# Kernel tuning notes

Hardware: AMD Instinct MI355X
Metric: run time of the kernel (lower is better)

## Reference

```python
import jax, jax.numpy as jnp
import numpy as np

B = 4
N_PER_B = 65536
N = B * N_PER_B
GROUP_SIZE = 64
ORDER = 9  # min bits to cover grid size 512
C0, C1, C2 = 64, 128, 128


def hilbert_encode(coors, order):
    """Skilling AxesToTranspose, vectorized over N points, 3 dims -> int32 code."""
    n = 3
    X = [coors[:, i].astype(jnp.int32) for i in range(n)]
    M = 1 << (order - 1)
    Q = M
    while Q > 1:
        P = Q - 1
        for i in range(n):
            cond = (X[i] & Q) != 0
            if i == 0:
                X[0] = jnp.where(cond, X[0] ^ P, X[0])
            else:
                t = (X[0] ^ X[i]) & P
                x0 = jnp.where(cond, X[0] ^ P, X[0] ^ t)
                xi = jnp.where(cond, X[i], X[i] ^ t)
                X[0], X[i] = x0, xi
        Q >>= 1
    for i in range(1, n):
        X[i] = X[i] ^ X[i - 1]
    t = jnp.zeros_like(X[0])
    Q = M
    while Q > 1:
        t = jnp.where((X[n - 1] & Q) != 0, t ^ (Q - 1), t)
        Q >>= 1
    X = [x ^ t for x in X]
    # interleave transposed bits MSB-first: code has 3*order bits (27 < 31, fits int32)
    code = jnp.zeros_like(X[0])
    for b in range(order - 1, -1, -1):
        for i in range(n):
            code = (code << 1) | ((X[i] >> b) & 1)
    return code


def _mapping_indices(vox_coors):
    """Two Hilbert orderings (normal + reversed coord axes); per-batch stable grouping."""
    batch = vox_coors[:, 0]
    c1 = vox_coors[:, 1:4]
    c2 = vox_coors[:, 3:0:-1]  # [0,3,2,1] reverse of the xyz columns
    code1 = hilbert_encode(c1, ORDER)
    code2 = hilbert_encode(c2, ORDER)
    ind1 = jnp.lexsort((code1, batch))  # batch-major, curve-order minor
    ind2 = jnp.lexsort((code2, batch))
    inv1 = jnp.argsort(ind1)
    ind12 = inv1[ind2]  # maps ordering-1 arrangement to ordering-2 arrangement
    return ind1, ind12


def _block(p, x, params):
    """VoxFormer-style block: center pts per group, pos-encode, gate feats, local attn, FFN."""
    Wpos, bpos, Wq, Wk, Wv, Wo, Wout = params
    C = Wq.shape[0]
    gs = GROUP_SIZE
    pg = p.reshape(-1, gs, 3)
    e = (pg - pg.mean(axis=1, keepdims=True)).reshape(-1, 3) @ Wpos + bpos  # [N,C]
    h = (x * e).reshape(-1, gs, C)  # [G,gs,C]
    q, k, v = h @ Wq, h @ Wk, h @ Wv
    scores = jnp.einsum('gqc,gkc->gqk', q, k) / jnp.sqrt(jnp.asarray(C, q.dtype))
    attn = jax.nn.softmax(scores, axis=-1)
    o = jnp.einsum('gqk,gkc->gqc', attn, v).reshape(-1, C) @ Wo
    return jax.nn.relu(o) @ Wout  # [N,C_out]


def setup_inputs() -> dict:
    key = jax.random.key(0)
    ks = jax.random.split(key, 20)
    bcol = jnp.repeat(jnp.arange(B, dtype=jnp.int32), N_PER_B)
    z = jax.random.randint(ks[0], (N,), 0, 64, dtype=jnp.int32)
    y = jax.random.randint(ks[1], (N,), 0, 512, dtype=jnp.int32)
    x = jax.random.randint(ks[2], (N,), 0, 512, dtype=jnp.int32)
    vox_coors = jnp.stack([bcol, z, y, x], axis=1)
    vox_numbs = jnp.full((B,), N_PER_B, dtype=jnp.int32)
    vox_feats = jax.random.normal(ks[3], (N, C0), dtype=jnp.float32)
    pts_coors = jax.random.normal(ks[4], (N, 3), dtype=jnp.float32)
    s = lambda k, shape: jax.random.normal(k, shape, dtype=jnp.float32) / np.float32(np.sqrt(shape[0]))
    return dict(
        vox_numbs=vox_numbs, vox_coors=vox_coors, vox_feats=vox_feats, pts_coors=pts_coors,
        Wpos1=s(ks[5], (3, C0)), bpos1=jnp.zeros((C0,), jnp.float32),
        Wq1=s(ks[6], (C0, C0)), Wk1=s(ks[7], (C0, C0)), Wv1=s(ks[8], (C0, C0)),
        Wo1=s(ks[9], (C0, C0)), Wout1=s(ks[10], (C0, C1)),
        Wpos2=s(ks[11], (3, C1)), bpos2=jnp.zeros((C1,), jnp.float32),
        Wq2=s(ks[12], (C1, C1)), Wk2=s(ks[13], (C1, C1)), Wv2=s(ks[14], (C1, C1)),
        Wo2=s(ks[15], (C1, C1)), Wout2=s(ks[16], (C1, C2)),
    )


def reference(vox_numbs, vox_coors, vox_feats, pts_coors,
              Wpos1, bpos1, Wq1, Wk1, Wv1, Wo1, Wout1,
              Wpos2, bpos2, Wq2, Wk2, Wv2, Wo2, Wout2):
    ind1, ind12 = _mapping_indices(vox_coors)
    params = ((Wpos1, bpos1, Wq1, Wk1, Wv1, Wo1, Wout1),
              (Wpos2, bpos2, Wq2, Wk2, Wv2, Wo2, Wout2))
    for ind, prm in zip((ind1, ind12), params):
        vox_feats = vox_feats[ind]
        pts_coors = pts_coors[ind]
        vox_coors = vox_coors[ind]
        vox_feats = _block(pts_coors, vox_feats, prm)
    return vox_feats, pts_coors, vox_coors, vox_numbs
```

## Files before the change

### kernel.cpp

```cpp
#include <hip/hip_runtime.h>

using u64 = unsigned long long;
typedef _Float16 f16;
using f16x8 = __attribute__((ext_vector_type(8))) _Float16;
using f16x4 = __attribute__((ext_vector_type(4))) _Float16;
using f32x4 = __attribute__((ext_vector_type(4))) float;

__device__ __forceinline__ int hilbert3(int X0, int X1, int X2) {
  #pragma unroll
  for (int Q = 256; Q > 1; Q >>= 1) {
    const int P = Q - 1;
    if (X0 & Q) X0 ^= P;
    int t1 = (X0 ^ X1) & P;
    if (X1 & Q) X0 ^= P; else { X0 ^= t1; X1 ^= t1; }
    int t2 = (X0 ^ X2) & P;
    if (X2 & Q) X0 ^= P; else { X0 ^= t2; X2 ^= t2; }
  }
  X1 ^= X0;
  X2 ^= X1;
  int t = 0;
  #pragma unroll
  for (int Q = 256; Q > 1; Q >>= 1) if (X2 & Q) t ^= (Q - 1);
  X0 ^= t; X1 ^= t; X2 ^= t;
  int code = 0;
  #pragma unroll
  for (int b = 8; b >= 0; b--)
    code = (code << 3) | (((X0 >> b) & 1) << 2) | (((X1 >> b) & 1) << 1) | ((X2 >> b) & 1);
  return code;
}

__global__ void encode_keys(const int* __restrict__ vox, u64* __restrict__ k1,
                            u64* __restrict__ k2, int n) {
  int i = blockIdx.x * blockDim.x + threadIdx.x;
  if (i >= n) return;
  int4 c = ((const int4*)vox)[i];
  unsigned code1 = (unsigned)hilbert3(c.y, c.z, c.w);
  unsigned code2 = (unsigned)hilbert3(c.w, c.z, c.y);
  u64 bb = ((u64)(unsigned)c.x << 45);
  k1[i] = bb | ((u64)code1 << 18) | (unsigned)i;
  k2[i] = bb | ((u64)code2 << 18) | (unsigned)i;
}

__device__ __forceinline__ void cswap(u64& a, u64& b, bool up) {
  if ((a > b) == up) { u64 t = a; a = b; b = t; }
}

__global__ __launch_bounds__(1024) void bitonic_tile_sort(u64* __restrict__ keys, int n) {
  keys += (size_t)blockIdx.y * n;
  __shared__ u64 s[2048];
  const int base = blockIdx.x * 2048;
  s[threadIdx.x]        = keys[base + threadIdx.x];
  s[threadIdx.x + 1024] = keys[base + threadIdx.x + 1024];
  __syncthreads();
  for (int k = 2; k <= 2048; k <<= 1) {
    for (int j = k >> 1; j >= 1; j >>= 1) {
      const int t = threadIdx.x;
      const int i = ((t & ~(j - 1)) << 1) | (t & (j - 1));
      const int l = i | j;
      const bool up = (((base + i) & k) == 0);
      u64 a = s[i], b = s[l];
      if ((a > b) == up) { s[i] = b; s[l] = a; }
      __syncthreads();
    }
  }
  keys[base + threadIdx.x]        = s[threadIdx.x];
  keys[base + threadIdx.x + 1024] = s[threadIdx.x + 1024];
}

__global__ void bitonic_g1(u64* __restrict__ keys, int j, int k, int n) {
  keys += (size_t)blockIdx.y * n;
  const int t = blockIdx.x * blockDim.x + threadIdx.x;
  const int i = ((t & ~(j - 1)) << 1) | (t & (j - 1));
  const int l = i | j;
  const bool up = ((i & k) == 0);
  u64 a = keys[i], b = keys[l];
  if ((a > b) == up) { keys[i] = b; keys[l] = a; }
}

__global__ void bitonic_g2(u64* __restrict__ keys, int j2, int k, int n) {
  keys += (size_t)blockIdx.y * n;
  const int t = blockIdx.x * blockDim.x + threadIdx.x;
  const int i = ((t & ~(j2 - 1)) << 2) | (t & (j2 - 1));
  const bool up = ((i & k) == 0);
  u64 x0 = keys[i], x1 = keys[i + j2], x2 = keys[i + 2 * j2], x3 = keys[i + 3 * j2];
  cswap(x0, x2, up); cswap(x1, x3, up);
  cswap(x0, x1, up); cswap(x2, x3, up);
  keys[i] = x0; keys[i + j2] = x1; keys[i + 2 * j2] = x2; keys[i + 3 * j2] = x3;
}

__global__ void bitonic_g3(u64* __restrict__ keys, int j4, int k, int n) {
  keys += (size_t)blockIdx.y * n;
  const int t = blockIdx.x * blockDim.x + threadIdx.x;
  const int i = ((t & ~(j4 - 1)) << 3) | (t & (j4 - 1));
  const bool up = ((i & k) == 0);
  u64 x[8];
  #pragma unroll
  for (int m = 0; m < 8; m++) x[m] = keys[i + m * j4];
  #pragma unroll
  for (int m = 0; m < 4; m++) cswap(x[m], x[m + 4], up);
  cswap(x[0], x[2], up); cswap(x[1], x[3], up);
  cswap(x[4], x[6], up); cswap(x[5], x[7], up);
  #pragma unroll
  for (int m = 0; m < 8; m += 2) cswap(x[m], x[m + 1], up);
  #pragma unroll
  for (int m = 0; m < 8; m++) keys[i + m * j4] = x[m];
}

__global__ __launch_bounds__(1024) void bitonic_tile_merge(u64* __restrict__ keys, int k, int n) {
  keys += (size_t)blockIdx.y * n;
  __shared__ u64 s[2048];
  const int base = blockIdx.x * 2048;
  s[threadIdx.x]        = keys[base + threadIdx.x];
  s[threadIdx.x + 1024] = keys[base + threadIdx.x + 1024];
  __syncthreads();
  const bool up = ((base & k) == 0);
  for (int j = 1024; j >= 1; j >>= 1) {
    const int t = threadIdx.x;
    const int i = ((t & ~(j - 1)) << 1) | (t & (j - 1));
    const int l = i | j;
    u64 a = s[i], b = s[l];
    if ((a > b) == up) { s[i] = b; s[l] = a; }
    __syncthreads();
  }
  keys[base + threadIdx.x]        = s[threadIdx.x];
  keys[base + threadIdx.x + 1024] = s[threadIdx.x + 1024];
}

__global__ void extract_inv_k(const u64* __restrict__ keys, int* __restrict__ ind,
                              int* __restrict__ inv, int n) {
  int t = blockIdx.x * blockDim.x + threadIdx.x;
  if (t >= n) return;
  int s = (int)(keys[t] & 0x3FFFFULL);
  ind[t] = s;
  inv[s] = t;
}

__global__ void make_g2_k(const u64* __restrict__ keys, const int* __restrict__ inv1,
                          int* __restrict__ ind2, int* __restrict__ g2, int n) {
  int t = blockIdx.x * blockDim.x + threadIdx.x;
  if (t >= n) return;
  int s = (int)(keys[t] & 0x3FFFFULL);
  ind2[t] = s;
  g2[t] = inv1[s];
}

__global__ void prep_all(const float* __restrict__ Wq1, const float* __restrict__ Wk1,
                         const float* __restrict__ Wv1, const float* __restrict__ Wo1,
                         const float* __restrict__ Wout1,
                         const float* __restrict__ Wq2, const float* __restrict__ Wk2,
                         const float* __restrict__ Wv2, const float* __restrict__ Wo2,
                         const float* __restrict__ Wout2,
                         f16* __restrict__ A1a, f16* __restrict__ A2a, f16* __restrict__ A3a,
                         f16* __restrict__ A1b, f16* __restrict__ A2b, f16* __restrict__ A3b) {
  const int idx = blockIdx.x * blockDim.x + threadIdx.x;
  if (idx < 4096) {
    const int a = idx >> 6, b = idx & 63;
    float s1 = 0.f, s2 = 0.f;
    for (int c = 0; c < 64; c++) {
      s1 = fmaf(Wq1[b * 64 + c], Wk1[a * 64 + c], s1);
      s2 = fmaf(Wv1[b * 64 + c], Wo1[c * 64 + a], s2);
    }
    A1a[idx] = (f16)(s1 * 0.125f);
    A2a[idx] = (f16)s2;
  }
  if (idx < 8192) {
    const int o = idx >> 6, c = idx & 63;
    A3a[idx] = (f16)Wout1[c * 128 + o];
  }
  {
    const int a = idx >> 7, b = idx & 127;
    float s1 = 0.f, s2 = 0.f;
    for (int c = 0; c < 128; c++) {
      s1 = fmaf(Wq2[b * 128 + c], Wk2[a * 128 + c], s1);
      s2 = fmaf(Wv2[b * 128 + c], Wo2[c * 128 + a], s2);
    }
    A1b[idx] = (f16)(s1 * 0.08838834764831845f);
    A2b[idx] = (f16)s2;
    A3b[idx] = (f16)Wout2[b * 128 + a];
  }
}


template<int M, int K, int AMODE>
__device__ __forceinline__ void gemmT(const f16* __restrict__ Ag, const f16* __restrict__ lA,
                                      const f16* __restrict__ lB, int w, int lane,
                                      f32x4 (&acc)[M / 64][4]) {
  constexpr int CT = M / 64;
  const int lr = lane & 15, lk = lane >> 4;
  #pragma unroll
  for (int ks = 0; ks < K / 32; ks++) {
    const int k0 = ks * 32 + lk * 8;
    f16x8 Af[CT];
    #pragma unroll
    for (int ct = 0; ct < CT; ct++) {
      const int c = lr + (w * CT + ct) * 16;
      if (AMODE == 0) {
        Af[ct] = *(const f16x8*)(Ag + (size_t)c * K + k0);
      } else if (AMODE == 1) {
        Af[ct] = *(const f16x8*)((const char*)lA + (((c * K + k0) * 2) ^ ((c & 7) << 4)));
      } else {
        f16x8 a;
        #pragma unroll
        for (int e = 0; e < 8; e++) {
          const int j = k0 + e;
          a[e] = *(const f16*)((const char*)lA + (((j * M + c) * 2) ^ ((j & 7) << 4)));
        }
        Af[ct] = a;
      }
    }
    f16x8 Bf[4];
    #pragma unroll
    for (int qt = 0; qt < 4; qt++) {
      const int q = lr + qt * 16;
      Bf[qt] = *(const f16x8*)((const char*)lB + (((q * K + k0) * 2) ^ ((q & 7) << 4)));
    }
    #pragma unroll
    for (int ct = 0; ct < CT; ct++)
      #pragma unroll
      for (int qt = 0; qt < 4; qt++)
        acc[ct][qt] = __builtin_amdgcn_mfma_f32_16x16x32_f16(Af[ct], Bf[qt], acc[ct][qt], 0, 0, 0);
  }
}

template<int M, bool RELU>
__device__ __forceinline__ void storeT16(f16* __restrict__ dst, int w, int lane,
                                         const f32x4 (&acc)[M / 64][4]) {
  constexpr int CT = M / 64;
  #pragma unroll
  for (int ct = 0; ct < CT; ct++)
    #pragma unroll
    for (int qt = 0; qt < 4; qt++) {
      const int q = (lane & 15) + qt * 16;
      const int c0 = (w * CT + ct) * 16 + (lane >> 4) * 4;
      f16x4 v;
      #pragma unroll
      for (int r = 0; r < 4; r++) {
        float x = acc[ct][qt][r];
        if (RELU) x = fmaxf(x, 0.f);
        v[r] = (f16)x;
      }
      *(f16x4*)((char*)dst + (((q * M + c0) * 2) ^ ((q & 7) << 4))) = v;
    }
}

template<int C, bool X16, bool OUT16>
__global__ __launch_bounds__(256, 3) void block_mfma(
    const int* __restrict__ idx_p, const int* __restrict__ idx_x,
    const float* __restrict__ pts, const void* __restrict__ xsrc,
    const float* __restrict__ Wpos, const float* __restrict__ bpos,
    const f16* __restrict__ A1, const f16* __restrict__ A2, const f16* __restrict__ A3,
    void* __restrict__ outp) {
  extern __shared__ char smem[];
  f16*   bufH = (f16*)smem;
  f16*   bufT = bufH + 64 * C;
  float* scF  = (float*)(bufT + 64 * C);

  const int g = blockIdx.x;
  const int t = threadIdx.x;
  const int lane = t & 63;
  const int w = t >> 6;

  {
    const int qr = t & 63;
    const int spr = idx_p[g * 64 + qr];
    float mx = pts[spr * 3 + 0], my = pts[spr * 3 + 1], mz = pts[spr * 3 + 2];
    #pragma unroll
    for (int o = 32; o > 0; o >>= 1) {
      mx += __shfl_xor(mx, o); my += __shfl_xor(my, o); mz += __shfl_xor(mz, o);
    }
    mx *= (1.f / 64.f); my *= (1.f / 64.f); mz *= (1.f / 64.f);

    const int q = t >> 2, qq = t & 3;
    const int sp = idx_p[g * 64 + q];
    const float d0 = pts[sp * 3 + 0] - mx;
    const float d1 = pts[sp * 3 + 1] - my;
    const float d2 = pts[sp * 3 + 2] - mz;
    const int sx = idx_x[g * 64 + q];
    #pragma unroll
    for (int i = 0; i < C / 32; i++) {
      const int c0 = qq * (C / 4) + i * 8;
      float xv[8];
      if (X16) {
        f16x8 xr = *(const f16x8*)((const f16*)xsrc + (size_t)sx * C + c0);
        #pragma unroll
        for (int j = 0; j < 8; j++) xv[j] = (float)xr[j];
      } else {
        float4 x0 = *(const float4*)((const float*)xsrc + (size_t)sx * C + c0);
        float4 x1 = *(const float4*)((const float*)xsrc + (size_t)sx * C + c0 + 4);
        xv[0] = x0.x; xv[1] = x0.y; xv[2] = x0.z; xv[3] = x0.w;
        xv[4] = x1.x; xv[5] = x1.y; xv[6] = x1.z; xv[7] = x1.w;
      }
      f16x8 hv;
      #pragma unroll
      for (int jj = 0; jj < 8; jj += 4) {
        const float4 w0 = *(const float4*)(Wpos + 0 * C + c0 + jj);
        const float4 w1 = *(const float4*)(Wpos + 1 * C + c0 + jj);
        const float4 w2 = *(const float4*)(Wpos + 2 * C + c0 + jj);
        const float4 bb = *(const float4*)(bpos + c0 + jj);
        hv[jj + 0] = (f16)(xv[jj + 0] * fmaf(d0, w0.x, fmaf(d1, w1.x, fmaf(d2, w2.x, bb.x))));
        hv[jj + 1] = (f16)(xv[jj + 1] * fmaf(d0, w0.y, fmaf(d1, w1.y, fmaf(d2, w2.y, bb.y))));
        hv[jj + 2] = (f16)(xv[jj + 2] * fmaf(d0, w0.z, fmaf(d1, w1.z, fmaf(d2, w2.z, bb.z))));
        hv[jj + 3] = (f16)(xv[jj + 3] * fmaf(d0, w0.w, fmaf(d1, w1.w, fmaf(d2, w2.w, bb.w))));
      }
      *(f16x8*)((char*)bufH + (((q * C + c0) * 2) ^ ((q & 7) << 4))) = hv;
    }
  }
  __syncthreads();

  {
    f32x4 acc[C / 64][4] = {};
    gemmT<C, C, 0>(A1, nullptr, bufH, w, lane, acc);
    storeT16<C, false>(bufT, w, lane, acc);
  }
  __syncthreads();

  {
    f32x4 acc[1][4] = {};
    gemmT<64, C, 1>(nullptr, bufH, bufT, w, lane, acc);
    #pragma unroll
    for (int qt = 0; qt < 4; qt++) {
      const int q = (lane & 15) + qt * 16;
      const int j0 = w * 16 + (lane >> 4) * 4;
      *(f32x4*)((char*)scF + (((q * 64 + j0) * 4) ^ ((q & 7) << 4))) = acc[0][qt];
    }
  }
  __syncthreads();

  {
    const int q = t >> 2, qq = t & 3;
    float v[16];
    float mxv = -3.0e38f;
    #pragma unroll
    for (int i = 0; i < 4; i++) {
      f32x4 x = *(const f32x4*)((const char*)scF + (((q * 64 + qq * 16 + i * 4) * 4) ^ ((q & 7) << 4)));
      v[i * 4 + 0] = x[0]; v[i * 4 + 1] = x[1]; v[i * 4 + 2] = x[2]; v[i * 4 + 3] = x[3];
      mxv = fmaxf(mxv, fmaxf(fmaxf(x[0], x[1]), fmaxf(x[2], x[3])));
    }
    mxv = fmaxf(mxv, __shfl_xor(mxv, 1));
    mxv = fmaxf(mxv, __shfl_xor(mxv, 2));
    float s = 0.f;
    #pragma unroll
    for (int i = 0; i < 16; i++) { v[i] = __expf(v[i] - mxv); s += v[i]; }
    s += __shfl_xor(s, 1);
    s += __shfl_xor(s, 2);
    const float inv = 1.f / s;
    __syncthreads();
    f16* at = (f16*)scF;
    #pragma unroll
    for (int hhalf = 0; hhalf < 2; hhalf++) {
      f16x8 pk;
      #pragma unroll
      for (int j = 0; j < 8; j++) pk[j] = (f16)(v[hhalf * 8 + j] * inv);
      *(f16x8*)((char*)at + (((q * 64 + qq * 16 + hhalf * 8) * 2) ^ ((q & 7) << 4))) = pk;
    }
  }
  __syncthreads();

  {
    f32x4 acc[C / 64][4] = {};
    gemmT<C, 64, 2>(nullptr, bufH, (const f16*)scF, w, lane, acc);
    storeT16<C, false>(bufT, w, lane, acc);
  }
  __syncthreads();

  {
    f32x4 acc[C / 64][4] = {};
    gemmT<C, C, 0>(A2, nullptr, bufT, w, lane, acc);
    storeT16<C, true>(bufH, w, lane, acc);
  }
  __syncthreads();

  {
    f32x4 acc[2][4] = {};
    gemmT<128, C, 0>(A3, nullptr, bufH, w, lane, acc);
    #pragma unroll
    for (int ct = 0; ct < 2; ct++)
      #pragma unroll
      for (int qt = 0; qt < 4; qt++) {
        const int q = (lane & 15) + qt * 16;
        const int o0 = (w * 2 + ct) * 16 + (lane >> 4) * 4;
        const size_t row = (size_t)g * 64 + q;
        if (OUT16) {
          f16x4 v;
          #pragma unroll
          for (int r = 0; r < 4; r++) v[r] = (f16)acc[ct][qt][r];
          *(f16x4*)((f16*)outp + row * 128 + o0) = v;
        } else {
          *(f32x4*)((float*)outp + row * 128 + o0) = acc[ct][qt];
        }
      }
  }
}

__global__ void finalize_k(const int* __restrict__ ind2, const float* __restrict__ pts,
                           const int* __restrict__ vox, const int* __restrict__ numbs,
                           float* __restrict__ out_pts, float* __restrict__ out_vox,
                           float* __restrict__ out_nb, int n, int B) {
  int t = blockIdx.x * blockDim.x + threadIdx.x;
  if (t < n) {
    const int s = ind2[t];
    out_pts[t * 3 + 0] = pts[s * 3 + 0];
    out_pts[t * 3 + 1] = pts[s * 3 + 1];
    out_pts[t * 3 + 2] = pts[s * 3 + 2];
    const int4 v = ((const int4*)vox)[s];
    out_vox[t * 4 + 0] = (float)v.x;
    out_vox[t * 4 + 1] = (float)v.y;
    out_vox[t * 4 + 2] = (float)v.z;
    out_vox[t * 4 + 3] = (float)v.w;
  }
  if (t < B) out_nb[t] = (float)numbs[t];
}

extern "C" void kernel_launch(void* const* d_in, const int* in_sizes, int n_in,
                              void* d_out, int out_size, void* d_ws, size_t ws_size,
                              hipStream_t stream) {
  const int*   vox_numbs = (const int*)d_in[0];
  const int*   vox_coors = (const int*)d_in[1];
  const float* vox_feats = (const float*)d_in[2];
  const float* pts_coors = (const float*)d_in[3];
  const float* Wpos1 = (const float*)d_in[4];
  const float* bpos1 = (const float*)d_in[5];
  const float* Wq1   = (const float*)d_in[6];
  const float* Wk1   = (const float*)d_in[7];
  const float* Wv1   = (const float*)d_in[8];
  const float* Wo1   = (const float*)d_in[9];
  const float* Wout1 = (const float*)d_in[10];
  const float* Wpos2 = (const float*)d_in[11];
  const float* bpos2 = (const float*)d_in[12];
  const float* Wq2   = (const float*)d_in[13];
  const float* Wk2   = (const float*)d_in[14];
  const float* Wv2   = (const float*)d_in[15];
  const float* Wo2   = (const float*)d_in[16];
  const float* Wout2 = (const float*)d_in[17];

  const int B = in_sizes[0];
  const int n = in_sizes[1] / 4;
  const int ngrp = n / 64;

  char* w = (char*)d_ws;
  auto alloc = [&](size_t bytes) {
    char* p = w;
    w += (bytes + 255) & ~(size_t)255;
    return p;
  };
  u64* keys    = (u64*)alloc((size_t)2 * n * 8);
  int* ind1    = (int*)alloc((size_t)n * 4);
  int* ind2    = (int*)alloc((size_t)n * 4);
  int* inv1    = (int*)alloc((size_t)n * 4);
  int* g2      = (int*)alloc((size_t)n * 4);
  f16* A1a     = (f16*)alloc(64 * 64 * 2);
  f16* A2a     = (f16*)alloc(64 * 64 * 2);
  f16* A3a     = (f16*)alloc(128 * 64 * 2);
  f16* A1b     = (f16*)alloc(128 * 128 * 2);
  f16* A2b     = (f16*)alloc(128 * 128 * 2);
  f16* A3b     = (f16*)alloc(128 * 128 * 2);
  f16* feats1  = (f16*)alloc((size_t)n * 128 * 2);
  u64* keys2   = keys + n;

  float* out_feats = (float*)d_out;
  float* out_pts   = out_feats + (size_t)n * 128;
  float* out_vox   = out_pts + (size_t)n * 3;
  float* out_nb    = out_vox + (size_t)n * 4;

  auto f64k  = block_mfma<64,  false, true>;
  auto f128k = block_mfma<128, true,  false>;
  hipFuncSetAttribute((const void*)f64k,  hipFuncAttributeMaxDynamicSharedMemorySize, 65536);
  hipFuncSetAttribute((const void*)f128k, hipFuncAttributeMaxDynamicSharedMemorySize, 65536);

  encode_keys<<<(n + 255) / 256, 256, 0, stream>>>(vox_coors, keys, keys2, n);
  prep_all<<<64, 256, 0, stream>>>(Wq1, Wk1, Wv1, Wo1, Wout1, Wq2, Wk2, Wv2, Wo2, Wout2,
                                   A1a, A2a, A3a, A1b, A2b, A3b);

  {
    const dim3 gt(n / 2048, 2);
    const dim3 g1(n / 512, 2), g2d(n / 1024, 2), g3d(n / 2048, 2);
    bitonic_tile_sort<<<gt, 1024, 0, stream>>>(keys, n);
    for (int k = 4096; k <= n; k <<= 1) {
      int levels = 0;
      for (int j = k >> 1; j >= 2048; j >>= 1) levels++;
      int j = k >> 1;
      while (levels >= 3) {
        bitonic_g3<<<g3d, 256, 0, stream>>>(keys, j >> 2, k, n);
        j >>= 3; levels -= 3;
      }
      if (levels == 2) { bitonic_g2<<<g2d, 256, 0, stream>>>(keys, j >> 1, k, n); j >>= 2; levels = 0; }
      else if (levels == 1) { bitonic_g1<<<g1, 256, 0, stream>>>(keys, j, k, n); j >>= 1; levels = 0; }
      bitonic_tile_merge<<<gt, 1024, 0, stream>>>(keys, k, n);
    }
  }
  extract_inv_k<<<(n + 255) / 256, 256, 0, stream>>>(keys, ind1, inv1, n);
  make_g2_k<<<(n + 255) / 256, 256, 0, stream>>>(keys2, inv1, ind2, g2, n);

  block_mfma<64, false, true><<<ngrp, 256, 32768, stream>>>(
      ind1, ind1, pts_coors, vox_feats, Wpos1, bpos1, A1a, A2a, A3a, feats1);
  block_mfma<128, true, false><<<ngrp, 256, 49152, stream>>>(
      ind2, g2, pts_coors, feats1, Wpos2, bpos2, A1b, A2b, A3b, out_feats);

  finalize_k<<<(n + 255) / 256, 256, 0, stream>>>(ind2, pts_coors, vox_coors, vox_numbs,
                                                  out_pts, out_vox, out_nb, n, B);
}
```

Baseline: 321.7 us.

## Fuse key encoding into 4096-tile sort, radix-16 merges, fp16 scores, pre-gathered points

Hilbert key encoding now happens inside a 4096-element shared-memory tile sort, and the global merge steps use a 16-way bitonic kernel. Both changes cut the number of kernel launches and global passes. Point coordinates are gathered once into sorted order and reused by both blocks, and the finalize work is folded into the g2 construction kernel. Inside the block kernel, the attention scores are stored as fp16 instead of fp32, which shrinks shared memory and allows higher occupancy (launch bounds raised from 3 to 4). The A1 fragments and the x loads are also hoisted into registers, at the cost of more register pressure and fp16 rounding of the scores.

```diff
diff --git a/kernel.cpp b/kernel.cpp
--- a/kernel.cpp
+++ b/kernel.cpp
@@ -29,52 +29,50 @@
   return code;
 }
 
-__global__ void encode_keys(const int* __restrict__ vox, u64* __restrict__ k1,
-                            u64* __restrict__ k2, int n) {
-  int i = blockIdx.x * blockDim.x + threadIdx.x;
-  if (i >= n) return;
-  int4 c = ((const int4*)vox)[i];
-  unsigned code1 = (unsigned)hilbert3(c.y, c.z, c.w);
-  unsigned code2 = (unsigned)hilbert3(c.w, c.z, c.y);
-  u64 bb = ((u64)(unsigned)c.x << 45);
-  k1[i] = bb | ((u64)code1 << 18) | (unsigned)i;
-  k2[i] = bb | ((u64)code2 << 18) | (unsigned)i;
-}
-
 __device__ __forceinline__ void cswap(u64& a, u64& b, bool up) {
   if ((a > b) == up) { u64 t = a; a = b; b = t; }
 }
 
-__global__ __launch_bounds__(1024) void bitonic_tile_sort(u64* __restrict__ keys, int n) {
-  keys += (size_t)blockIdx.y * n;
-  __shared__ u64 s[2048];
-  const int base = blockIdx.x * 2048;
-  s[threadIdx.x]        = keys[base + threadIdx.x];
-  s[threadIdx.x + 1024] = keys[base + threadIdx.x + 1024];
-  __syncthreads();
-  for (int k = 2; k <= 2048; k <<= 1) {
+__global__ __launch_bounds__(1024) void sort_tile0(const int* __restrict__ vox,
+                                                   u64* __restrict__ keys, int n) {
+  __shared__ u64 s[4096];
+  const int base = blockIdx.x * 4096;
+  const int which = blockIdx.y;
+  u64* kout = keys + (size_t)which * n;
+  #pragma unroll
+  for (int m = 0; m < 4; m++) {
+    const int i = base + threadIdx.x + m * 1024;
+    int4 c = ((const int4*)vox)[i];
+    unsigned code = which == 0 ? (unsigned)hilbert3(c.y, c.z, c.w)
+                               : (unsigned)hilbert3(c.w, c.z, c.y);
+    s[threadIdx.x + m * 1024] = ((u64)(unsigned)c.x << 45) | ((u64)code << 18) | (unsigned)i;
+  }
+  __syncthreads();
+  for (int k = 2; k <= 4096; k <<= 1) {
     for (int j = k >> 1; j >= 1; j >>= 1) {
-      const int t = threadIdx.x;
-      const int i = ((t & ~(j - 1)) << 1) | (t & (j - 1));
-      const int l = i | j;
-      const bool up = (((base + i) & k) == 0);
-      u64 a = s[i], b = s[l];
-      if ((a > b) == up) { s[i] = b; s[l] = a; }
+      #pragma unroll
+      for (int m = 0; m < 2; m++) {
+        const int p = threadIdx.x + m * 1024;
+        const int i = ((p & ~(j - 1)) << 1) | (p & (j - 1));
+        const bool up = (((base + i) & k) == 0);
+        u64 a = s[i], b = s[i | j];
+        if ((a > b) == up) { s[i] = b; s[i | j] = a; }
+      }
       __syncthreads();
     }
   }
-  keys[base + threadIdx.x]        = s[threadIdx.x];
-  keys[base + threadIdx.x + 1024] = s[threadIdx.x + 1024];
+  #pragma unroll
+  for (int m = 0; m < 4; m++)
+    kout[base + threadIdx.x + m * 1024] = s[threadIdx.x + m * 1024];
 }
 
 __global__ void bitonic_g1(u64* __restrict__ keys, int j, int k, int n) {
   keys += (size_t)blockIdx.y * n;
   const int t = blockIdx.x * blockDim.x + threadIdx.x;
   const int i = ((t & ~(j - 1)) << 1) | (t & (j - 1));
-  const int l = i | j;
   const bool up = ((i & k) == 0);
-  u64 a = keys[i], b = keys[l];
-  if ((a > b) == up) { keys[i] = b; keys[l] = a; }
+  u64 a = keys[i], b = keys[i | j];
+  if ((a > b) == up) { keys[i] = b; keys[i | j] = a; }
 }
 
 __global__ void bitonic_g2(u64* __restrict__ keys, int j2, int k, int n) {
@@ -106,42 +104,83 @@
   for (int m = 0; m < 8; m++) keys[i + m * j4] = x[m];
 }
 
-__global__ __launch_bounds__(1024) void bitonic_tile_merge(u64* __restrict__ keys, int k, int n) {
+__global__ void bitonic_g4(u64* __restrict__ keys, int j8, int k, int n) {
   keys += (size_t)blockIdx.y * n;
-  __shared__ u64 s[2048];
-  const int base = blockIdx.x * 2048;
-  s[threadIdx.x]        = keys[base + threadIdx.x];
-  s[threadIdx.x + 1024] = keys[base + threadIdx.x + 1024];
+  const int t = blockIdx.x * blockDim.x + threadIdx.x;
+  const int i = ((t & ~(j8 - 1)) << 4) | (t & (j8 - 1));
+  const bool up = ((i & k) == 0);
+  u64 x[16];
+  #pragma unroll
+  for (int m = 0; m < 16; m++) x[m] = keys[i + m * j8];
+  #pragma unroll
+  for (int m = 0; m < 8; m++) cswap(x[m], x[m + 8], up);
+  #pragma unroll
+  for (int h = 0; h < 16; h += 8)
+    #pragma unroll
+    for (int m = 0; m < 4; m++) cswap(x[h + m], x[h + m + 4], up);
+  #pragma unroll
+  for (int h = 0; h < 16; h += 4) { cswap(x[h], x[h + 2], up); cswap(x[h + 1], x[h + 3], up); }
+  #pragma unroll
+  for (int m = 0; m < 16; m += 2) cswap(x[m], x[m + 1], up);
+  #pragma unroll
+  for (int m = 0; m < 16; m++) keys[i + m * j8] = x[m];
+}
+
+__global__ __launch_bounds__(1024) void merge_tile4(u64* __restrict__ keys, int k, int n) {
+  keys += (size_t)blockIdx.y * n;
+  __shared__ u64 s[4096];
+  const int base = blockIdx.x * 4096;
+  #pragma unroll
+  for (int m = 0; m < 4; m++)
+    s[threadIdx.x + m * 1024] = keys[base + threadIdx.x + m * 1024];
   __syncthreads();
   const bool up = ((base & k) == 0);
-  for (int j = 1024; j >= 1; j >>= 1) {
-    const int t = threadIdx.x;
-    const int i = ((t & ~(j - 1)) << 1) | (t & (j - 1));
-    const int l = i | j;
-    u64 a = s[i], b = s[l];
-    if ((a > b) == up) { s[i] = b; s[l] = a; }
+  for (int j = 2048; j >= 1; j >>= 1) {
+    #pragma unroll
+    for (int m = 0; m < 2; m++) {
+      const int p = threadIdx.x + m * 1024;
+      const int i = ((p & ~(j - 1)) << 1) | (p & (j - 1));
+      u64 a = s[i], b = s[i | j];
+      if ((a > b) == up) { s[i] = b; s[i | j] = a; }
+    }
     __syncthreads();
   }
-  keys[base + threadIdx.x]        = s[threadIdx.x];
-  keys[base + threadIdx.x + 1024] = s[threadIdx.x + 1024];
-}
-
-__global__ void extract_inv_k(const u64* __restrict__ keys, int* __restrict__ ind,
-                              int* __restrict__ inv, int n) {
+  #pragma unroll
+  for (int m = 0; m < 4; m++)
+    keys[base + threadIdx.x + m * 1024] = s[threadIdx.x + m * 1024];
+}
+
+__global__ void extract_inv_k(const u64* __restrict__ keys, const float* __restrict__ pts,
+                              int* __restrict__ ind, int* __restrict__ inv,
+                              float* __restrict__ pts1p, int n) {
   int t = blockIdx.x * blockDim.x + threadIdx.x;
   if (t >= n) return;
   int s = (int)(keys[t] & 0x3FFFFULL);
   ind[t] = s;
   inv[s] = t;
-}
-
-__global__ void make_g2_k(const u64* __restrict__ keys, const int* __restrict__ inv1,
-                          int* __restrict__ ind2, int* __restrict__ g2, int n) {
+  pts1p[t * 3 + 0] = pts[s * 3 + 0];
+  pts1p[t * 3 + 1] = pts[s * 3 + 1];
+  pts1p[t * 3 + 2] = pts[s * 3 + 2];
+}
+
+__global__ void finish_k(const u64* __restrict__ keys2, const int* __restrict__ inv1,
+                         int* __restrict__ g2, const float* __restrict__ pts,
+                         const int* __restrict__ vox, const int* __restrict__ numbs,
+                         float* __restrict__ out_pts, float* __restrict__ out_vox,
+                         float* __restrict__ out_nb, int n, int B) {
   int t = blockIdx.x * blockDim.x + threadIdx.x;
   if (t >= n) return;
-  int s = (int)(keys[t] & 0x3FFFFULL);
-  ind2[t] = s;
+  int s = (int)(keys2[t] & 0x3FFFFULL);
   g2[t] = inv1[s];
+  out_pts[t * 3 + 0] = pts[s * 3 + 0];
+  out_pts[t * 3 + 1] = pts[s * 3 + 1];
+  out_pts[t * 3 + 2] = pts[s * 3 + 2];
+  const int4 v = ((const int4*)vox)[s];
+  out_vox[t * 4 + 0] = (float)v.x;
+  out_vox[t * 4 + 1] = (float)v.y;
+  out_vox[t * 4 + 2] = (float)v.z;
+  out_vox[t * 4 + 3] = (float)v.w;
+  if (t < B) out_nb[t] = (float)numbs[t];
 }
 
 __global__ void prep_all(const float* __restrict__ Wq1, const float* __restrict__ Wk1,
@@ -180,7 +219,6 @@
   }
 }
 
-
 template<int M, int K, int AMODE>
 __device__ __forceinline__ void gemmT(const f16* __restrict__ Ag, const f16* __restrict__ lA,
                                       const f16* __restrict__ lB, int w, int lane,
@@ -244,52 +282,65 @@
 }
 
 template<int C, bool X16, bool OUT16>
-__global__ __launch_bounds__(256, 3) void block_mfma(
-    const int* __restrict__ idx_p, const int* __restrict__ idx_x,
-    const float* __restrict__ pts, const void* __restrict__ xsrc,
+__global__ __launch_bounds__(256, 4) void block_mfma(
+    const int* __restrict__ idx_x, const float* __restrict__ ptsP,
+    const void* __restrict__ xsrc,
     const float* __restrict__ Wpos, const float* __restrict__ bpos,
     const f16* __restrict__ A1, const f16* __restrict__ A2, const f16* __restrict__ A3,
     void* __restrict__ outp) {
+  constexpr int CT = C / 64;
   extern __shared__ char smem[];
-  f16*   bufH = (f16*)smem;
-  f16*   bufT = bufH + 64 * C;
-  float* scF  = (float*)(bufT + 64 * C);
+  f16* bufH = (f16*)smem;
+  f16* bufT = bufH + 64 * C;
+  f16* scH  = bufT + 64 * C;
 
   const int g = blockIdx.x;
   const int t = threadIdx.x;
   const int lane = t & 63;
   const int w = t >> 6;
-
-  {
-    const int qr = t & 63;
-    const int spr = idx_p[g * 64 + qr];
-    float mx = pts[spr * 3 + 0], my = pts[spr * 3 + 1], mz = pts[spr * 3 + 2];
+  const int lr = lane & 15, lk = lane >> 4;
+
+  f16x8 A1f[C / 32][CT];
+  #pragma unroll
+  for (int ks = 0; ks < C / 32; ks++)
+    #pragma unroll
+    for (int ct = 0; ct < CT; ct++)
+      A1f[ks][ct] = *(const f16x8*)(A1 + (size_t)(lr + (w * CT + ct) * 16) * C + ks * 32 + lk * 8);
+
+  const int q = t >> 2, qq = t & 3;
+  const int sx = idx_x[g * 64 + q];
+  float xv[C / 4];
+  if (X16) {
+    #pragma unroll
+    for (int i = 0; i < C / 32; i++) {
+      f16x8 xr = *(const f16x8*)((const f16*)xsrc + (size_t)sx * C + qq * (C / 4) + i * 8);
+      #pragma unroll
+      for (int j = 0; j < 8; j++) xv[i * 8 + j] = (float)xr[j];
+    }
+  } else {
+    #pragma unroll
+    for (int i = 0; i < C / 16; i++) {
+      float4 x0 = *(const float4*)((const float*)xsrc + (size_t)sx * C + qq * (C / 4) + i * 4);
+      xv[i * 4 + 0] = x0.x; xv[i * 4 + 1] = x0.y; xv[i * 4 + 2] = x0.z; xv[i * 4 + 3] = x0.w;
+    }
+  }
+
+  {
+    float mx = ptsP[(g * 64 + lane) * 3 + 0];
+    float my = ptsP[(g * 64 + lane) * 3 + 1];
+    float mz = ptsP[(g * 64 + lane) * 3 + 2];
     #pragma unroll
     for (int o = 32; o > 0; o >>= 1) {
       mx += __shfl_xor(mx, o); my += __shfl_xor(my, o); mz += __shfl_xor(mz, o);
     }
     mx *= (1.f / 64.f); my *= (1.f / 64.f); mz *= (1.f / 64.f);
 
-    const int q = t >> 2, qq = t & 3;
-    const int sp = idx_p[g * 64 + q];
-    const float d0 = pts[sp * 3 + 0] - mx;
-    const float d1 = pts[sp * 3 + 1] - my;
-    const float d2 = pts[sp * 3 + 2] - mz;
-    const int sx = idx_x[g * 64 + q];
+    const float d0 = ptsP[(g * 64 + q) * 3 + 0] - mx;
+    const float d1 = ptsP[(g * 64 + q) * 3 + 1] - my;
+    const float d2 = ptsP[(g * 64 + q) * 3 + 2] - mz;
     #pragma unroll
     for (int i = 0; i < C / 32; i++) {
       const int c0 = qq * (C / 4) + i * 8;
-      float xv[8];
-      if (X16) {
-        f16x8 xr = *(const f16x8*)((const f16*)xsrc + (size_t)sx * C + c0);
-        #pragma unroll
-        for (int j = 0; j < 8; j++) xv[j] = (float)xr[j];
-      } else {
-        float4 x0 = *(const float4*)((const float*)xsrc + (size_t)sx * C + c0);
-        float4 x1 = *(const float4*)((const float*)xsrc + (size_t)sx * C + c0 + 4);
-        xv[0] = x0.x; xv[1] = x0.y; xv[2] = x0.z; xv[3] = x0.w;
-        xv[4] = x1.x; xv[5] = x1.y; xv[6] = x1.z; xv[7] = x1.w;
-      }
       f16x8 hv;
       #pragma unroll
       for (int jj = 0; jj < 8; jj += 4) {
@@ -297,10 +348,10 @@
         const float4 w1 = *(const float4*)(Wpos + 1 * C + c0 + jj);
         const float4 w2 = *(const float4*)(Wpos + 2 * C + c0 + jj);
         const float4 bb = *(const float4*)(bpos + c0 + jj);
-        hv[jj + 0] = (f16)(xv[jj + 0] * fmaf(d0, w0.x, fmaf(d1, w1.x, fmaf(d2, w2.x, bb.x))));
-        hv[jj + 1] = (f16)(xv[jj + 1] * fmaf(d0, w0.y, fmaf(d1, w1.y, fmaf(d2, w2.y, bb.y))));
-        hv[jj + 2] = (f16)(xv[jj + 2] * fmaf(d0, w0.z, fmaf(d1, w1.z, fmaf(d2, w2.z, bb.z))));
-        hv[jj + 3] = (f16)(xv[jj + 3] * fmaf(d0, w0.w, fmaf(d1, w1.w, fmaf(d2, w2.w, bb.w))));
+        hv[jj + 0] = (f16)(xv[i * 8 + jj + 0] * fmaf(d0, w0.x, fmaf(d1, w1.x, fmaf(d2, w2.x, bb.x))));
+        hv[jj + 1] = (f16)(xv[i * 8 + jj + 1] * fmaf(d0, w0.y, fmaf(d1, w1.y, fmaf(d2, w2.y, bb.y))));
+        hv[jj + 2] = (f16)(xv[i * 8 + jj + 2] * fmaf(d0, w0.z, fmaf(d1, w1.z, fmaf(d2, w2.z, bb.z))));
+        hv[jj + 3] = (f16)(xv[i * 8 + jj + 3] * fmaf(d0, w0.w, fmaf(d1, w1.w, fmaf(d2, w2.w, bb.w))));
       }
       *(f16x8*)((char*)bufH + (((q * C + c0) * 2) ^ ((q & 7) << 4))) = hv;
     }
@@ -308,8 +359,22 @@
   __syncthreads();
 
   {
-    f32x4 acc[C / 64][4] = {};
-    gemmT<C, C, 0>(A1, nullptr, bufH, w, lane, acc);
+    f32x4 acc[CT][4] = {};
+    #pragma unroll
+    for (int ks = 0; ks < C / 32; ks++) {
+      const int k0 = ks * 32 + lk * 8;
+      f16x8 Bf[4];
+      #pragma unroll
+      for (int qt = 0; qt < 4; qt++) {
+        const int qr = lr + qt * 16;
+        Bf[qt] = *(const f16x8*)((const char*)bufH + (((qr * C + k0) * 2) ^ ((qr & 7) << 4)));
+      }
+      #pragma unroll
+      for (int ct = 0; ct < CT; ct++)
+        #pragma unroll
+        for (int qt = 0; qt < 4; qt++)
+          acc[ct][qt] = __builtin_amdgcn_mfma_f32_16x16x32_f16(A1f[ks][ct], Bf[qt], acc[ct][qt], 0, 0, 0);
+    }
     storeT16<C, false>(bufT, w, lane, acc);
   }
   __syncthreads();
@@ -319,22 +384,27 @@
     gemmT<64, C, 1>(nullptr, bufH, bufT, w, lane, acc);
     #pragma unroll
     for (int qt = 0; qt < 4; qt++) {
-      const int q = (lane & 15) + qt * 16;
-      const int j0 = w * 16 + (lane >> 4) * 4;
-      *(f32x4*)((char*)scF + (((q * 64 + j0) * 4) ^ ((q & 7) << 4))) = acc[0][qt];
-    }
-  }
-  __syncthreads();
-
-  {
-    const int q = t >> 2, qq = t & 3;
+      const int qr = lr + qt * 16;
+      const int j0 = w * 16 + lk * 4;
+      f16x4 v;
+      #pragma unroll
+      for (int r = 0; r < 4; r++) v[r] = (f16)acc[0][qt][r];
+      *(f16x4*)((char*)scH + (((qr * 64 + j0) * 2) ^ ((qr & 7) << 4))) = v;
+    }
+  }
+  __syncthreads();
+
+  {
     float v[16];
     float mxv = -3.0e38f;
     #pragma unroll
-    for (int i = 0; i < 4; i++) {
-      f32x4 x = *(const f32x4*)((const char*)scF + (((q * 64 + qq * 16 + i * 4) * 4) ^ ((q & 7) << 4)));
-      v[i * 4 + 0] = x[0]; v[i * 4 + 1] = x[1]; v[i * 4 + 2] = x[2]; v[i * 4 + 3] = x[3];
-      mxv = fmaxf(mxv, fmaxf(fmaxf(x[0], x[1]), fmaxf(x[2], x[3])));
+    for (int i = 0; i < 2; i++) {
+      f16x8 x8 = *(const f16x8*)((const char*)scH + (((q * 64 + qq * 16 + i * 8) * 2) ^ ((q & 7) << 4)));
+      #pragma unroll
+      for (int j = 0; j < 8; j++) {
+        v[i * 8 + j] = (float)x8[j];
+        mxv = fmaxf(mxv, v[i * 8 + j]);
+      }
     }
     mxv = fmaxf(mxv, __shfl_xor(mxv, 1));
     mxv = fmaxf(mxv, __shfl_xor(mxv, 2));
@@ -344,27 +414,25 @@
     s += __shfl_xor(s, 1);
     s += __shfl_xor(s, 2);
     const float inv = 1.f / s;
-    __syncthreads();
-    f16* at = (f16*)scF;
-    #pragma unroll
-    for (int hhalf = 0; hhalf < 2; hhalf++) {
+    #pragma unroll
+    for (int i = 0; i < 2; i++) {
       f16x8 pk;
       #pragma unroll
-      for (int j = 0; j < 8; j++) pk[j] = (f16)(v[hhalf * 8 + j] * inv);
-      *(f16x8*)((char*)at + (((q * 64 + qq * 16 + hhalf * 8) * 2) ^ ((q & 7) << 4))) = pk;
-    }
-  }
-  __syncthreads();
-
-  {
-    f32x4 acc[C / 64][4] = {};
-    gemmT<C, 64, 2>(nullptr, bufH, (const f16*)scF, w, lane, acc);
+      for (int j = 0; j < 8; j++) pk[j] = (f16)(v[i * 8 + j] * inv);
+      *(f16x8*)((char*)scH + (((q * 64 + qq * 16 + i * 8) * 2) ^ ((q & 7) << 4))) = pk;
+    }
+  }
+  __syncthreads();
+
+  {
+    f32x4 acc[CT][4] = {};
+    gemmT<C, 64, 2>(nullptr, bufH, scH, w, lane, acc);
     storeT16<C, false>(bufT, w, lane, acc);
   }
   __syncthreads();
 
   {
-    f32x4 acc[C / 64][4] = {};
+    f32x4 acc[CT][4] = {};
     gemmT<C, C, 0>(A2, nullptr, bufT, w, lane, acc);
     storeT16<C, true>(bufH, w, lane, acc);
   }
@@ -377,9 +445,9 @@
     for (int ct = 0; ct < 2; ct++)
       #pragma unroll
       for (int qt = 0; qt < 4; qt++) {
-        const int q = (lane & 15) + qt * 16;
+        const int qr = (lane & 15) + qt * 16;
         const int o0 = (w * 2 + ct) * 16 + (lane >> 4) * 4;
-        const size_t row = (size_t)g * 64 + q;
+        const size_t row = (size_t)g * 64 + qr;
         if (OUT16) {
           f16x4 v;
           #pragma unroll
@@ -390,25 +458,6 @@
         }
       }
   }
-}
-
-__global__ void finalize_k(const int* __restrict__ ind2, const float* __restrict__ pts,
-                           const int* __restrict__ vox, const int* __restrict__ numbs,
-                           float* __restrict__ out_pts, float* __restrict__ out_vox,
-                           float* __restrict__ out_nb, int n, int B) {
-  int t = blockIdx.x * blockDim.x + threadIdx.x;
-  if (t < n) {
-    const int s = ind2[t];
-    out_pts[t * 3 + 0] = pts[s * 3 + 0];
-    out_pts[t * 3 + 1] = pts[s * 3 + 1];
-    out_pts[t * 3 + 2] = pts[s * 3 + 2];
-    const int4 v = ((const int4*)vox)[s];
-    out_vox[t * 4 + 0] = (float)v.x;
-    out_vox[t * 4 + 1] = (float)v.y;
-    out_vox[t * 4 + 2] = (float)v.z;
-    out_vox[t * 4 + 3] = (float)v.w;
-  }
-  if (t < B) out_nb[t] = (float)numbs[t];
 }
 
 extern "C" void kernel_launch(void* const* d_in, const int* in_sizes, int n_in,
@@ -445,9 +494,9 @@
   };
   u64* keys    = (u64*)alloc((size_t)2 * n * 8);
   int* ind1    = (int*)alloc((size_t)n * 4);
-  int* ind2    = (int*)alloc((size_t)n * 4);
   int* inv1    = (int*)alloc((size_t)n * 4);
   int* g2      = (int*)alloc((size_t)n * 4);
+  float* pts1p = (float*)alloc((size_t)n * 3 * 4);
   f16* A1a     = (f16*)alloc(64 * 64 * 2);
   f16* A2a     = (f16*)alloc(64 * 64 * 2);
   f16* A3a     = (f16*)alloc(128 * 64 * 2);
@@ -467,35 +516,33 @@
   hipFuncSetAttribute((const void*)f64k,  hipFuncAttributeMaxDynamicSharedMemorySize, 65536);
   hipFuncSetAttribute((const void*)f128k, hipFuncAttributeMaxDynamicSharedMemorySize, 65536);
 
-  encode_keys<<<(n + 255) / 256, 256, 0, stream>>>(vox_coors, keys, keys2, n);
+  sort_tile0<<<dim3(n / 4096, 2), 1024, 0, stream>>>(vox_coors, keys, n);
   prep_all<<<64, 256, 0, stream>>>(Wq1, Wk1, Wv1, Wo1, Wout1, Wq2, Wk2, Wv2, Wo2, Wout2,
                                    A1a, A2a, A3a, A1b, A2b, A3b);
 
   {
-    const dim3 gt(n / 2048, 2);
-    const dim3 g1(n / 512, 2), g2d(n / 1024, 2), g3d(n / 2048, 2);
-    bitonic_tile_sort<<<gt, 1024, 0, stream>>>(keys, n);
-    for (int k = 4096; k <= n; k <<= 1) {
+    const dim3 gm(n / 4096, 2);
+    const dim3 d1(n / 512, 2), d2(n / 1024, 2), d3(n / 2048, 2), d4(n / 4096, 2);
+    for (int k = 8192; k <= n; k <<= 1) {
       int levels = 0;
-      for (int j = k >> 1; j >= 2048; j >>= 1) levels++;
+      for (int j = k >> 1; j >= 4096; j >>= 1) levels++;
       int j = k >> 1;
-      while (levels >= 3) {
-        bitonic_g3<<<g3d, 256, 0, stream>>>(keys, j >> 2, k, n);
-        j >>= 3; levels -= 3;
-      }
-      if (levels == 2) { bitonic_g2<<<g2d, 256, 0, stream>>>(keys, j >> 1, k, n); j >>= 2; levels = 0; }
-      else if (levels == 1) { bitonic_g1<<<g1, 256, 0, stream>>>(keys, j, k, n); j >>= 1; levels = 0; }
-      bitonic_tile_merge<<<gt, 1024, 0, stream>>>(keys, k, n);
-    }
-  }
-  extract_inv_k<<<(n + 255) / 256, 256, 0, stream>>>(keys, ind1, inv1, n);
-  make_g2_k<<<(n + 255) / 256, 256, 0, stream>>>(keys2, inv1, ind2, g2, n);
-
-  block_mfma<64, false, true><<<ngrp, 256, 32768, stream>>>(
-      ind1, ind1, pts_coors, vox_feats, Wpos1, bpos1, A1a, A2a, A3a, feats1);
-  block_mfma<128, true, false><<<ngrp, 256, 49152, stream>>>(
-      ind2, g2, pts_coors, feats1, Wpos2, bpos2, A1b, A2b, A3b, out_feats);
-
-  finalize_k<<<(n + 255) / 256, 256, 0, stream>>>(ind2, pts_coors, vox_coors, vox_numbs,
-                                                  out_pts, out_vox, out_nb, n, B);
-}
+      while (levels >= 4) {
+        bitonic_g4<<<d4, 256, 0, stream>>>(keys, j >> 3, k, n);
+        j >>= 4; levels -= 4;
+      }
+      if (levels == 3)      { bitonic_g3<<<d3, 256, 0, stream>>>(keys, j >> 2, k, n); }
+      else if (levels == 2) { bitonic_g2<<<d2, 256, 0, stream>>>(keys, j >> 1, k, n); }
+      else if (levels == 1) { bitonic_g1<<<d1, 256, 0, stream>>>(keys, j, k, n); }
+      merge_tile4<<<gm, 1024, 0, stream>>>(keys, k, n);
+    }
+  }
+  extract_inv_k<<<(n + 255) / 256, 256, 0, stream>>>(keys, pts_coors, ind1, inv1, pts1p, n);
+  finish_k<<<(n + 255) / 256, 256, 0, stream>>>(keys2, inv1, g2, pts_coors, vox_coors,
+                                                vox_numbs, out_pts, out_vox, out_nb, n, B);
+
+  block_mfma<64, false, true><<<ngrp, 256, 24576, stream>>>(
+      ind1, pts1p, vox_feats, Wpos1, bpos1, A1a, A2a, A3a, feats1);
+  block_mfma<128, true, false><<<ngrp, 256, 40960, stream>>>(
+      g2, out_pts, feats1, Wpos2, bpos2, A1b, A2b, A3b, out_feats);
+}
```

Result: slower. 331.5 us (+3.1%).
